# Kernel optimization log

Measured on AMD Instinct MI355X. Metric: run time of the kernel, lower is better.

The kernel has to match this reference:

```python
import jax, jax.numpy as jnp
import numpy as np
import math

D_MODEL = 1024
N_HEADS = 16
DK = D_MODEL // N_HEADS


def setup_inputs() -> dict:
    key = jax.random.key(0)
    kx, kqkv, kproj = jax.random.split(key, 3)
    B, T = 4, 2048
    x = jax.random.normal(kx, (B, T, D_MODEL), dtype=jnp.float32)
    # torch Linear weight is [out, in]; y = x @ W.T
    W_qkv = jax.random.normal(kqkv, (3 * D_MODEL, D_MODEL), dtype=jnp.float32) * (1.0 / math.sqrt(D_MODEL))
    W_proj = jax.random.normal(kproj, (D_MODEL, D_MODEL), dtype=jnp.float32) * (1.0 / math.sqrt(D_MODEL))
    return {"x": x, "W_qkv": W_qkv, "W_proj": W_proj}


def reference(x, W_qkv, W_proj):
    B, T, D = x.shape
    qkv = jnp.einsum("btd,ed->bte", x, W_qkv)  # [B,T,3D]
    q, k, v = jnp.split(qkv, 3, axis=-1)
    # [B,T,D] -> [B,H,T,dk]
    def heads(t):
        return t.reshape(B, T, N_HEADS, DK).transpose(0, 2, 1, 3)
    q, k, v = heads(q), heads(k), heads(v)
    scale = 1.0 / math.sqrt(DK)
    att = jnp.einsum("bhqd,bhkd->bhqk", q, k) * scale  # [B,H,T,T]
    att = jax.nn.softmax(att, axis=-1)
    out = jnp.einsum("bhqk,bhkd->bhqd", att, v)  # [B,H,T,dk]
    out = out.transpose(0, 2, 1, 3).reshape(B, T, D)
    return jnp.einsum("btd,ed->bte", out, W_proj)
```

## Files before the change

kernel.cpp:

```cpp
#include <hip/hip_runtime.h>
#include <hip/hip_bf16.h>

#define D_MODEL 1024
#define N_HEADS 16
#define DK 64
#define B_SZ 4
#define T_SEQ 2048
#define M_ROWS (B_SZ * T_SEQ)
#define QK_SCALE_LOG2 0.18033688f

typedef short bf16x8 __attribute__((ext_vector_type(8)));
typedef float f32x4  __attribute__((ext_vector_type(4)));

__device__ inline unsigned short f32_to_bf16(float f) {
    union { float f; unsigned int u; } v; v.f = f;
    unsigned int r = v.u + 0x7fff + ((v.u >> 16) & 1);
    return (unsigned short)(r >> 16);
}
__device__ inline unsigned int pack_bf16x2(float a, float b) {
    __hip_bfloat162 t = __float22bfloat162_rn(make_float2(a, b));
    union { __hip_bfloat162 v; unsigned int u; } c; c.v = t;
    return c.u;
}

__global__ __launch_bounds__(256) void cast_bf16(
    const float* __restrict__ src, unsigned short* __restrict__ dst,
    int n, int nscaled, float s)
{
    for (int i = (blockIdx.x * 256 + threadIdx.x) * 4; i < n;
         i += gridDim.x * 256 * 4) {
        float4 v = *(const float4*)(src + i);
        const float sc = (i < nscaled) ? s : 1.0f;
        ushort4 h;
        h.x = f32_to_bf16(v.x * sc); h.y = f32_to_bf16(v.y * sc);
        h.z = f32_to_bf16(v.z * sc); h.w = f32_to_bf16(v.w * sc);
        *(ushort4*)(dst + i) = h;
    }
}

template <typename OutT>
__global__ __launch_bounds__(256) void gemm_bf16_nt(
    const unsigned short* __restrict__ A, const unsigned short* __restrict__ B,
    OutT* __restrict__ C, int M, int N, int K)
{
    __shared__ __align__(16) unsigned short sA[128 * 32];
    __shared__ __align__(16) unsigned short sB[128 * 32];

    const int t    = threadIdx.x;
    const int wave = t >> 6;
    const int lane = t & 63;
    const int l15  = lane & 15;
    const int quad = lane >> 4;
    const int m0   = blockIdx.y * 128;
    const int n0   = blockIdx.x * 128;

    const unsigned short* gplane = (wave < 2) ? A : B;
    unsigned short* lplane = (wave < 2) ? sA : sB;
    const int row0 = ((wave < 2) ? m0 : n0) + (wave & 1) * 64;
    const int lds0 = (wave & 1) * 2048;
    const unsigned short* gbase =
        gplane + (size_t)(row0 + (lane >> 2)) * K + (lane & 3) * 8;

    f32x4 acc[4][4];
#pragma unroll
    for (int i = 0; i < 4; ++i)
#pragma unroll
        for (int j = 0; j < 4; ++j) acc[i][j] = (f32x4){0.f, 0.f, 0.f, 0.f};

    const int wr = (wave >> 1) * 64;
    const int wc = (wave & 1) * 64;

    for (int k0 = 0; k0 < K; k0 += 32) {
#pragma unroll
        for (int i = 0; i < 4; ++i) {
            __builtin_amdgcn_global_load_lds(
                (const __attribute__((address_space(1))) unsigned int*)
                    (gbase + k0 + (size_t)i * 16 * K),
                (__attribute__((address_space(3))) unsigned int*)
                    (lplane + lds0 + i * 512),
                16, 0, 0);
        }
        __syncthreads();

        bf16x8 a[4], b[4];
#pragma unroll
        for (int f = 0; f < 4; ++f) {
            a[f] = *(const bf16x8*)&sA[(wr + f * 16 + l15) * 32 + quad * 8];
            b[f] = *(const bf16x8*)&sB[(wc + f * 16 + l15) * 32 + quad * 8];
        }
#pragma unroll
        for (int mi = 0; mi < 4; ++mi)
#pragma unroll
            for (int ni = 0; ni < 4; ++ni)
                acc[mi][ni] = __builtin_amdgcn_mfma_f32_16x16x32_bf16(
                    a[mi], b[ni], acc[mi][ni], 0, 0, 0);
        __syncthreads();
    }

#pragma unroll
    for (int mi = 0; mi < 4; ++mi)
#pragma unroll
        for (int r = 0; r < 4; ++r) {
            OutT* crow =
                C + (size_t)(m0 + wr + mi * 16 + quad * 4 + r) * N + n0 + wc + l15;
#pragma unroll
            for (int ni = 0; ni < 4; ++ni) {
                if constexpr (sizeof(OutT) == 2)
                    crow[ni * 16] = (OutT)f32_to_bf16(acc[mi][ni][r]);
                else
                    crow[ni * 16] = (OutT)acc[mi][ni][r];
            }
        }
}

__global__ __launch_bounds__(256) void prep_vt(
    const unsigned short* __restrict__ qkvb, unsigned short* __restrict__ vt)
{
    __shared__ unsigned short VT_s[64][264];
    const int t  = threadIdx.x;
    const int b  = blockIdx.z, h = blockIdx.y;
    const int t0 = blockIdx.x * 256;
    const unsigned short* vb = qkvb + (size_t)(b * T_SEQ) * (3 * D_MODEL)
                               + 2 * D_MODEL + h * DK;
#pragma unroll
    for (int it = 0; it < 16; ++it) {
        const int trow = (t >> 4) + it * 16;
        const int dk0  = (t & 15) * 4;
        ushort4 v = *(const ushort4*)(vb + (size_t)(t0 + trow) * (3 * D_MODEL) + dk0);
        VT_s[dk0 + 0][trow] = v.x; VT_s[dk0 + 1][trow] = v.y;
        VT_s[dk0 + 2][trow] = v.z; VT_s[dk0 + 3][trow] = v.w;
    }
    __syncthreads();
    const int row = t >> 2;
    const int c0w = (t & 3) * 64;
    unsigned short* dst = vt + ((size_t)(b * N_HEADS + h) * DK + row) * T_SEQ + t0 + c0w;
#pragma unroll
    for (int i = 0; i < 8; ++i) {
        const int lp8   = c0w + i * 8;
        const int sbase = (lp8 & ~31) + ((lp8 >> 3) & 3) * 4;
        ushort4 a  = *(const ushort4*)&VT_s[row][sbase];
        ushort4 b4 = *(const ushort4*)&VT_s[row][sbase + 16];
        union { ushort4 p[2]; uint4 v; } pk;
        pk.p[0] = a; pk.p[1] = b4;
        *(uint4*)(dst + i * 8) = pk.v;
    }
}

__global__ __launch_bounds__(256) void attn_mfma(
    const unsigned short* __restrict__ qkvb,
    const unsigned short* __restrict__ vt,
    unsigned short* __restrict__ ob)
{
    __shared__ __align__(16) unsigned short Ksw[2][128 * 64];
    __shared__ __align__(16) unsigned short Vsw[2][64 * 128];

    const int t    = threadIdx.x;
    const int wave = t >> 6;
    const int lane = t & 63;
    const int l15  = t & 15;
    const int quad = lane >> 4;
    const int swz  = l15 & 7;

    const int b  = blockIdx.z;
    const int h  = blockIdx.y;
    const int q0 = blockIdx.x * 128;

    bf16x8 qa[2][2];
#pragma unroll
    for (int qs = 0; qs < 2; ++qs) {
        const unsigned short* qrow =
            qkvb + ((size_t)(b * T_SEQ) + q0 + wave * 32 + qs * 16 + l15)
                   * (3 * D_MODEL) + h * DK;
        qa[qs][0] = *(const bf16x8*)(qrow + quad * 8);
        qa[qs][1] = *(const bf16x8*)(qrow + 32 + quad * 8);
    }

    f32x4 O[2][4], Lacc[2];
#pragma unroll
    for (int qs = 0; qs < 2; ++qs) {
        Lacc[qs] = (f32x4){0.f, 0.f, 0.f, 0.f};
#pragma unroll
        for (int nd = 0; nd < 4; ++nd) O[qs][nd] = (f32x4){0.f, 0.f, 0.f, 0.f};
    }

    const short one_bf = (short)0x3F80;
    const bf16x8 ones8 = {one_bf, one_bf, one_bf, one_bf,
                          one_bf, one_bf, one_bf, one_bf};

    const unsigned short* kbase =
        qkvb + (size_t)(b * T_SEQ) * (3 * D_MODEL) + D_MODEL + h * DK;
    const unsigned short* vbase = vt + (size_t)(b * N_HEADS + h) * DK * T_SEQ;

    const int krl  = wave * 32 + (lane >> 3);
    const int kcol = ((lane & 7) ^ (lane >> 3)) * 8;
    const int vrl = wave * 16 + (lane >> 4);
    const int vsw = lane & 15;

#pragma unroll
    for (int i = 0; i < 4; ++i) {
        const int rk = krl + i * 8;
        __builtin_amdgcn_global_load_lds(
            (const __attribute__((address_space(1))) unsigned int*)
                (kbase + (size_t)rk * (3 * D_MODEL) + kcol),
            (__attribute__((address_space(3))) unsigned int*)
                (&Ksw[0][(wave * 4 + i) * 512]),
            16, 0, 0);
        const int rv = vrl + i * 4;
        const int vc = (((vsw & 7) ^ (rv & 7)) | (vsw & 8)) * 8;
        __builtin_amdgcn_global_load_lds(
            (const __attribute__((address_space(1))) unsigned int*)
                (vbase + (size_t)rv * T_SEQ + vc),
            (__attribute__((address_space(3))) unsigned int*)
                (&Vsw[0][(wave * 4 + i) * 512]),
            16, 0, 0);
    }

    const int NT = T_SEQ / 128;
    for (int tile = 0; tile < NT; ++tile) {
        __syncthreads();

        if (tile + 1 < NT) {
            const int c0n = (tile + 1) * 128;
            const int nb  = (tile + 1) & 1;
#pragma unroll
            for (int i = 0; i < 4; ++i) {
                const int rk = krl + i * 8;
                __builtin_amdgcn_global_load_lds(
                    (const __attribute__((address_space(1))) unsigned int*)
                        (kbase + (size_t)(c0n + rk) * (3 * D_MODEL) + kcol),
                    (__attribute__((address_space(3))) unsigned int*)
                        (&Ksw[nb][(wave * 4 + i) * 512]),
                    16, 0, 0);
                const int rv = vrl + i * 4;
                const int vc = (((vsw & 7) ^ (rv & 7)) | (vsw & 8)) * 8;
                __builtin_amdgcn_global_load_lds(
                    (const __attribute__((address_space(1))) unsigned int*)
                        (vbase + (size_t)rv * T_SEQ + c0n + vc),
                    (__attribute__((address_space(3))) unsigned int*)
                        (&Vsw[nb][(wave * 4 + i) * 512]),
                    16, 0, 0);
            }
        }

        const int cb = tile & 1;
#pragma unroll
        for (int half = 0; half < 2; ++half) {
            f32x4 S[2][4];
#pragma unroll
            for (int qs = 0; qs < 2; ++qs)
#pragma unroll
                for (int nf = 0; nf < 4; ++nf) S[qs][nf] = (f32x4){0.f, 0.f, 0.f, 0.f};
#pragma unroll
            for (int ks = 0; ks < 2; ++ks) {
                const int ch = ks * 4 + quad;
#pragma unroll
                for (int nf = 0; nf < 4; ++nf) {
                    const int row = half * 64 + nf * 16 + l15;
                    const bf16x8 kf =
                        *(const bf16x8*)&Ksw[cb][row * 64 + ((ch ^ swz) * 8)];
                    S[0][nf] = __builtin_amdgcn_mfma_f32_16x16x32_bf16(
                        kf, qa[0][ks], S[0][nf], 0, 0, 0);
                    S[1][nf] = __builtin_amdgcn_mfma_f32_16x16x32_bf16(
                        kf, qa[1][ks], S[1][nf], 0, 0, 0);
                }
            }

#pragma unroll
            for (int gl = 0; gl < 2; ++gl) {
                bf16x8 pf[2];
#pragma unroll
                for (int qs = 0; qs < 2; ++qs) {
                    union { uint4 u; bf16x8 v; } cv;
                    const f32x4 s0 = S[qs][2 * gl];
                    const f32x4 s1 = S[qs][2 * gl + 1];
                    cv.u.x = pack_bf16x2(__builtin_amdgcn_exp2f(s0[0]),
                                         __builtin_amdgcn_exp2f(s0[1]));
                    cv.u.y = pack_bf16x2(__builtin_amdgcn_exp2f(s0[2]),
                                         __builtin_amdgcn_exp2f(s0[3]));
                    cv.u.z = pack_bf16x2(__builtin_amdgcn_exp2f(s1[0]),
                                         __builtin_amdgcn_exp2f(s1[1]));
                    cv.u.w = pack_bf16x2(__builtin_amdgcn_exp2f(s1[2]),
                                         __builtin_amdgcn_exp2f(s1[3]));
                    pf[qs] = cv.v;
                }
                const int g = half * 2 + gl;
                const int c = g * 4 + quad;
                const int vo = (((c & 7) ^ swz) | (c & 8)) * 8;
#pragma unroll
                for (int nd = 0; nd < 4; ++nd) {
                    const bf16x8 vb =
                        *(const bf16x8*)&Vsw[cb][(nd * 16 + l15) * 128 + vo];
                    O[0][nd] = __builtin_amdgcn_mfma_f32_16x16x32_bf16(
                        pf[0], vb, O[0][nd], 0, 0, 0);
                    O[1][nd] = __builtin_amdgcn_mfma_f32_16x16x32_bf16(
                        pf[1], vb, O[1][nd], 0, 0, 0);
                }
                Lacc[0] = __builtin_amdgcn_mfma_f32_16x16x32_bf16(
                    pf[0], ones8, Lacc[0], 0, 0, 0);
                Lacc[1] = __builtin_amdgcn_mfma_f32_16x16x32_bf16(
                    pf[1], ones8, Lacc[1], 0, 0, 0);
            }
        }
    }

#pragma unroll
    for (int qs = 0; qs < 2; ++qs)
#pragma unroll
        for (int r = 0; r < 4; ++r) {
            const float invl = 1.0f / Lacc[qs][r];
            const size_t rowbase =
                ((size_t)(b * T_SEQ) + q0 + wave * 32 + qs * 16 + quad * 4 + r)
                * D_MODEL + h * DK + l15;
#pragma unroll
            for (int nd = 0; nd < 4; ++nd)
                ob[rowbase + nd * 16] = f32_to_bf16(O[qs][nd][r] * invl);
        }
}

extern "C" void kernel_launch(void* const* d_in, const int* in_sizes, int n_in,
                              void* d_out, int out_size, void* d_ws, size_t ws_size,
                              hipStream_t stream)
{
    const float* x      = (const float*)d_in[0];
    const float* W_qkv  = (const float*)d_in[1];
    const float* W_proj = (const float*)d_in[2];
    float* out = (float*)d_out;

    const size_t XN = (size_t)M_ROWS * D_MODEL;
    const size_t WQ = (size_t)3 * D_MODEL * D_MODEL;
    const size_t WP = (size_t)D_MODEL * D_MODEL;
    unsigned short* xb   = (unsigned short*)d_ws;
    unsigned short* wqb  = xb + XN;
    unsigned short* wpb  = wqb + WQ;
    unsigned short* qkvb = wpb + WP;
    unsigned short* vtb  = qkvb + (size_t)M_ROWS * 3 * D_MODEL;
    unsigned short* ab   = xb;

    dim3 blk(256);
    cast_bf16<<<512, blk, 0, stream>>>(x, xb, (int)XN, 0, 1.0f);
    cast_bf16<<<256, blk, 0, stream>>>(W_qkv, wqb, (int)WQ,
                                       D_MODEL * D_MODEL, QK_SCALE_LOG2);
    cast_bf16<<<128, blk, 0, stream>>>(W_proj, wpb, (int)WP, 0, 1.0f);

    gemm_bf16_nt<unsigned short>
        <<<dim3(3 * D_MODEL / 128, M_ROWS / 128), blk, 0, stream>>>(
        xb, wqb, qkvb, M_ROWS, 3 * D_MODEL, D_MODEL);

    prep_vt<<<dim3(T_SEQ / 256, N_HEADS, B_SZ), blk, 0, stream>>>(qkvb, vtb);
    attn_mfma<<<dim3(T_SEQ / 128, N_HEADS, B_SZ), blk, 0, stream>>>(
        qkvb, vtb, ab);

    gemm_bf16_nt<float>
        <<<dim3(D_MODEL / 128, M_ROWS / 128), blk, 0, stream>>>(
        ab, wpb, out, M_ROWS, D_MODEL, D_MODEL);
}
```

Before: 307.4 us.

## Pre-swizzle V into MFMA fragment order and read it directly from global memory

```diff
diff --git a/kernel.cpp b/kernel.cpp
--- a/kernel.cpp
+++ b/kernel.cpp
@@ -116,14 +116,14 @@
 __global__ __launch_bounds__(256) void prep_vt(
     const unsigned short* __restrict__ qkvb, unsigned short* __restrict__ vt)
 {
-    __shared__ unsigned short VT_s[64][264];
+    __shared__ unsigned short VT_s[64][132];
     const int t  = threadIdx.x;
     const int b  = blockIdx.z, h = blockIdx.y;
-    const int t0 = blockIdx.x * 256;
+    const int t0 = blockIdx.x * 128;
     const unsigned short* vb = qkvb + (size_t)(b * T_SEQ) * (3 * D_MODEL)
                                + 2 * D_MODEL + h * DK;
 #pragma unroll
-    for (int it = 0; it < 16; ++it) {
+    for (int it = 0; it < 8; ++it) {
         const int trow = (t >> 4) + it * 16;
         const int dk0  = (t & 15) * 4;
         ushort4 v = *(const ushort4*)(vb + (size_t)(t0 + trow) * (3 * D_MODEL) + dk0);
@@ -131,28 +131,30 @@
         VT_s[dk0 + 2][trow] = v.z; VT_s[dk0 + 3][trow] = v.w;
     }
     __syncthreads();
-    const int row = t >> 2;
-    const int c0w = (t & 3) * 64;
-    unsigned short* dst = vt + ((size_t)(b * N_HEADS + h) * DK + row) * T_SEQ + t0 + c0w;
-#pragma unroll
-    for (int i = 0; i < 8; ++i) {
-        const int lp8   = c0w + i * 8;
-        const int sbase = (lp8 & ~31) + ((lp8 >> 3) & 3) * 4;
-        ushort4 a  = *(const ushort4*)&VT_s[row][sbase];
-        ushort4 b4 = *(const ushort4*)&VT_s[row][sbase + 16];
+
+    const int c     = t >> 4;
+    const int p8    = c * 8;
+    const int sbase = (p8 & ~31) + ((p8 >> 3) & 3) * 4;
+    unsigned short* dst =
+        vt + (((size_t)((b * N_HEADS + h) * (T_SEQ / 128) + blockIdx.x) * 16 + c)
+              * 64) * 8;
+#pragma unroll
+    for (int dd = 0; dd < 4; ++dd) {
+        const int d = (t & 15) + dd * 16;
+        ushort4 a  = *(const ushort4*)&VT_s[d][sbase];
+        ushort4 b4 = *(const ushort4*)&VT_s[d][sbase + 16];
         union { ushort4 p[2]; uint4 v; } pk;
         pk.p[0] = a; pk.p[1] = b4;
-        *(uint4*)(dst + i * 8) = pk.v;
-    }
-}
-
-__global__ __launch_bounds__(256) void attn_mfma(
+        *(uint4*)(dst + d * 8) = pk.v;
+    }
+}
+
+__global__ __launch_bounds__(256, 4) void attn_mfma(
     const unsigned short* __restrict__ qkvb,
     const unsigned short* __restrict__ vt,
     unsigned short* __restrict__ ob)
 {
     __shared__ __align__(16) unsigned short Ksw[2][128 * 64];
-    __shared__ __align__(16) unsigned short Vsw[2][64 * 128];
 
     const int t    = threadIdx.x;
     const int wave = t >> 6;
@@ -189,12 +191,11 @@
 
     const unsigned short* kbase =
         qkvb + (size_t)(b * T_SEQ) * (3 * D_MODEL) + D_MODEL + h * DK;
-    const unsigned short* vbase = vt + (size_t)(b * N_HEADS + h) * DK * T_SEQ;
+    const unsigned short* vbase =
+        vt + (size_t)(b * N_HEADS + h) * DK * T_SEQ;
 
     const int krl  = wave * 32 + (lane >> 3);
     const int kcol = ((lane & 7) ^ (lane >> 3)) * 8;
-    const int vrl = wave * 16 + (lane >> 4);
-    const int vsw = lane & 15;
 
 #pragma unroll
     for (int i = 0; i < 4; ++i) {
@@ -205,14 +206,6 @@
             (__attribute__((address_space(3))) unsigned int*)
                 (&Ksw[0][(wave * 4 + i) * 512]),
             16, 0, 0);
-        const int rv = vrl + i * 4;
-        const int vc = (((vsw & 7) ^ (rv & 7)) | (vsw & 8)) * 8;
-        __builtin_amdgcn_global_load_lds(
-            (const __attribute__((address_space(1))) unsigned int*)
-                (vbase + (size_t)rv * T_SEQ + vc),
-            (__attribute__((address_space(3))) unsigned int*)
-                (&Vsw[0][(wave * 4 + i) * 512]),
-            16, 0, 0);
     }
 
     const int NT = T_SEQ / 128;
@@ -231,18 +224,11 @@
                     (__attribute__((address_space(3))) unsigned int*)
                         (&Ksw[nb][(wave * 4 + i) * 512]),
                     16, 0, 0);
-                const int rv = vrl + i * 4;
-                const int vc = (((vsw & 7) ^ (rv & 7)) | (vsw & 8)) * 8;
-                __builtin_amdgcn_global_load_lds(
-                    (const __attribute__((address_space(1))) unsigned int*)
-                        (vbase + (size_t)rv * T_SEQ + c0n + vc),
-                    (__attribute__((address_space(3))) unsigned int*)
-                        (&Vsw[nb][(wave * 4 + i) * 512]),
-                    16, 0, 0);
             }
         }
 
         const int cb = tile & 1;
+        const unsigned short* vtile = vbase + (size_t)tile * (16 * 64 * 8);
 #pragma unroll
         for (int half = 0; half < 2; ++half) {
             f32x4 S[2][4];
@@ -284,12 +270,11 @@
                     pf[qs] = cv.v;
                 }
                 const int g = half * 2 + gl;
-                const int c = g * 4 + quad;
-                const int vo = (((c & 7) ^ swz) | (c & 8)) * 8;
+                const unsigned short* vptr =
+                    vtile + (size_t)(g * 4 + quad) * 512 + l15 * 8;
 #pragma unroll
                 for (int nd = 0; nd < 4; ++nd) {
-                    const bf16x8 vb =
-                        *(const bf16x8*)&Vsw[cb][(nd * 16 + l15) * 128 + vo];
+                    const bf16x8 vb = *(const bf16x8*)(vptr + nd * 128);
                     O[0][nd] = __builtin_amdgcn_mfma_f32_16x16x32_bf16(
                         pf[0], vb, O[0][nd], 0, 0, 0);
                     O[1][nd] = __builtin_amdgcn_mfma_f32_16x16x32_bf16(
@@ -346,7 +331,7 @@
         <<<dim3(3 * D_MODEL / 128, M_ROWS / 128), blk, 0, stream>>>(
         xb, wqb, qkvb, M_ROWS, 3 * D_MODEL, D_MODEL);
 
-    prep_vt<<<dim3(T_SEQ / 256, N_HEADS, B_SZ), blk, 0, stream>>>(qkvb, vtb);
+    prep_vt<<<dim3(T_SEQ / 128, N_HEADS, B_SZ), blk, 0, stream>>>(qkvb, vtb);
     attn_mfma<<<dim3(T_SEQ / 128, N_HEADS, B_SZ), blk, 0, stream>>>(
         qkvb, vtb, ab);
 
```

Result: no change. 309.2 us (+0.6%).
